# Optimization experiments

Measured on AMD Instinct MI355X. Metric: run time of the kernel, lower is better.

## Reference

```python
import jax, jax.numpy as jnp
from jax import lax
import numpy as np

E = 3            # num_experts
HEAD_CONV = 128  # head_conv
N_HEADS = 3      # hm, wh, reg
HEAD_CH = 2      # channels per head
BN_EPS = 1e-5


def _conv(x, w, stride, pad, groups=1):
    return lax.conv_general_dilated(
        x, w, (stride, stride), [(pad, pad), (pad, pad)],
        feature_group_count=groups,
        dimension_numbers=('NCHW', 'OIHW', 'NCHW'))


def _maxpool3s2p1(x):
    return lax.reduce_window(
        x, -jnp.inf, lax.max, (1, 1, 3, 3), (1, 1, 2, 2),
        ((0, 0), (0, 0), (1, 1), (1, 1)))


def setup_inputs() -> dict:
    key = jax.random.key(0)
    ks = jax.random.split(key, 8)
    B, C, T, H, W = 16, 3, 5, 384, 384
    s = 0.05
    inp = {
        'x': jax.random.normal(ks[0], (B, C, T, H, W), jnp.float32),
        # gating network params
        'g_conv_w': jax.random.normal(ks[1], (64, C * T, 7, 7), jnp.float32) * s,
        'g_bn_gamma': jnp.ones((64,), jnp.float32),
        'g_bn_beta': jnp.zeros((64,), jnp.float32),
        'g_bn_mean': jnp.zeros((64,), jnp.float32),
        'g_bn_var': jnp.ones((64,), jnp.float32),
        'g_fc_w': jax.random.normal(ks[2], (E, 64), jnp.float32) * s,
        'g_fc_b': jnp.zeros((E,), jnp.float32),
        # frozen expert params (stacked over expert dim E)
        'e_conv1_w': jax.random.normal(ks[3], (E, 64, C * T, 7, 7), jnp.float32) * s,
        'e_conv1_b': jnp.zeros((E, 64), jnp.float32),
        'e_head_w1': jax.random.normal(ks[4], (E, N_HEADS * HEAD_CONV, 64, 3, 3), jnp.float32) * s,
        'e_head_b1': jnp.zeros((E, N_HEADS * HEAD_CONV), jnp.float32),
        'e_head_w2': jax.random.normal(ks[5], (E, N_HEADS * HEAD_CH, HEAD_CONV, 1, 1), jnp.float32) * s,
        'e_head_b2': jnp.zeros((E, N_HEADS * HEAD_CH), jnp.float32),
    }
    return inp


def reference(x, g_conv_w, g_bn_gamma, g_bn_beta, g_bn_mean, g_bn_var,
              g_fc_w, g_fc_b, e_conv1_w, e_conv1_b,
              e_head_w1, e_head_b1, e_head_w2, e_head_b2):
    b, c, t, h, w = x.shape
    xr = x.reshape(b, c * t, h, w)

    # ---- ConvGatingNetwork ----
    f = _conv(xr, g_conv_w, 2, 3)                                  # [B,64,H/2,W/2]
    inv = g_bn_gamma / jnp.sqrt(g_bn_var + BN_EPS)
    f = f * inv[None, :, None, None] + (g_bn_beta - g_bn_mean * inv)[None, :, None, None]
    f = jax.nn.relu(f)
    f = _maxpool3s2p1(f)                                           # [B,64,H/4,W/4]
    feat = f.mean(axis=(2, 3))                                     # [B,64]
    logits = feat @ g_fc_w.T + g_fc_b                              # [B,E]
    idx = jnp.argmax(logits, axis=1)                               # top-1
    onehot = jax.nn.one_hot(idx, E, dtype=logits.dtype)            # [B,E]
    density = onehot.mean(axis=0)
    density_proxy = jax.nn.softmax(logits, axis=1).mean(axis=0)
    aux_loss = (density * density_proxy).sum() * E

    # ---- Experts (frozen DSFNet stand-in), computed densely then gathered ----
    def expert(cw, cb, hw1, hb1, hw2, hb2):
        y = jax.nn.relu(_conv(xr, cw, 4, 3) + cb[None, :, None, None])       # [B,64,H/4,W/4]
        y = jax.nn.relu(_conv(y, hw1, 1, 1) + hb1[None, :, None, None])      # [B,384,h,w]
        y = _conv(y, hw2, 1, 0, groups=N_HEADS) + hb2[None, :, None, None]   # [B,6,h,w]
        return y

    out_all = jax.vmap(expert)(e_conv1_w, e_conv1_b, e_head_w1, e_head_b1,
                               e_head_w2, e_head_b2)               # [E,B,6,h,w]
    out_all = lax.stop_gradient(out_all)  # experts frozen + torch.no_grad
    out = jnp.einsum('be,ebchw->bchw', onehot, out_all)            # per-sample top-1 gather
    return out, 0.01 * aux_loss
```

## Files before the change

kernel.cpp:

```cpp
#include <hip/hip_runtime.h>
#include <math.h>

#define BB 16
#define CIN 15
#define HW 384
#define XPL 147456
#define NX 35389440
#define PH 96
#define GW 192
#define YP 98
#define Y1IPL (98*98*64)
#define OUT_ELEMS (BB*6*PH*PH)

#define OFF_WG   0
#define OFF_WE1  122880
#define OFF_WH   491520
#define OFF_GSH  1818624
#define OFF_FEAT 1818880
#define OFF_IDX  1822976
#define OFF_CBUF 2097152

typedef __attribute__((ext_vector_type(8))) short short8;
typedef __attribute__((ext_vector_type(4))) float floatx4;
typedef __attribute__((ext_vector_type(4))) unsigned int uintx4;
typedef __attribute__((ext_vector_type(2))) unsigned int uintx2;

__device__ __forceinline__ unsigned bf16rne(float f) {
  unsigned u = __float_as_uint(f);
  unsigned r = ((u >> 16) & 1u) + 0x7FFFu;
  return (u + r) >> 16;
}
__device__ __forceinline__ float bf2f(unsigned short s) {
  return __uint_as_float(((unsigned)s) << 16);
}

__global__ __launch_bounds__(256) void k_prep(
    const float* __restrict__ g_conv_w, const float* __restrict__ e_conv1_w,
    const float* __restrict__ e_head_w1,
    const float* __restrict__ gamma, const float* __restrict__ var,
    const float* __restrict__ beta,  const float* __restrict__ mean,
    unsigned char* __restrict__ wsb)
{
  int i = blockIdx.x * 256 + threadIdx.x;
  unsigned short* Wg  = (unsigned short*)(wsb + OFF_WG);
  unsigned short* We1 = (unsigned short*)(wsb + OFF_WE1);
  unsigned short* Wh  = (unsigned short*)(wsb + OFF_WH);
  float* gsh = (float*)(wsb + OFF_GSH);
  if (i < 61440) {
    int j = i & 7, lane = (i >> 3) & 63, mtc = i >> 9;
    int mt = mtc & 3, c = mtc >> 2, ic = c >> 1, h = c & 1;
    int oc = mt * 16 + (lane & 15), q = lane >> 4;
    int ky = 4 * h + q, kx = j;
    float v = 0.f;
    if (ky < 7 && kx < 7) v = g_conv_w[oc * 735 + ic * 49 + ky * 7 + kx];
    float inv = gamma[oc] * rsqrtf(var[oc] + 1e-5f);
    Wg[i] = (unsigned short)bf16rne(v * inv);
  } else if (i < 245760) {
    int r = i - 61440;
    int e = r / 61440, r2 = r % 61440;
    int j = r2 & 7, lane = (r2 >> 3) & 63, mtc = r2 >> 9;
    int mt = mtc & 3, c = mtc >> 2, ic = c >> 1, h = c & 1;
    int oc = mt * 16 + (lane & 15), q = lane >> 4;
    int ky = 4 * h + q, kx = j;
    float v = 0.f;
    if (ky < 7 && kx < 7) v = e_conv1_w[(e * 64 + oc) * 735 + ic * 49 + ky * 7 + kx];
    We1[r] = (unsigned short)bf16rne(v);
  } else if (i < 909312) {
    int r = i - 245760;
    int e = r / 221184, r2 = r % 221184;
    int j = r2 & 7, lane = (r2 >> 3) & 63, mtc = r2 >> 9;
    int mt = mtc % 24, chunk = mtc / 24;
    int kk = chunk >> 1, ih = chunk & 1;
    int oc = mt * 16 + (lane & 15), q = lane >> 4;
    int ic = ih * 32 + q * 8 + j;
    Wh[r] = (unsigned short)bf16rne(e_head_w1[((e * 384 + oc) * 64 + ic) * 9 + kk]);
  } else if (i < 909376) {
    int oc = i - 909312;
    float inv = gamma[oc] * rsqrtf(var[oc] + 1e-5f);
    gsh[oc] = beta[oc] - mean[oc] * inv;
  }
}

__global__ __launch_bounds__(256) void k_gconv(
    const float* __restrict__ x, const unsigned short* __restrict__ Wg,
    const float* __restrict__ gsh, unsigned short* __restrict__ Cbuf)
{
  const int t = threadIdx.x, w = t >> 6, lane = t & 63, q = lane >> 4, ln = lane & 15;
  const int px0 = blockIdx.x * 16, py0 = blockIdx.y * 16, b = blockIdx.z;
  const int iy0 = 2 * py0 - 3, ix0 = 2 * px0 - 3;

  __shared__ unsigned tilU[11400];

  {
    const bool edge = (blockIdx.x == 0) | (blockIdx.x == 11) |
                      (blockIdx.y == 0) | (blockIdx.y == 11);
    const int xbase = b * CIN * XPL;
    if (!edge) {
      for (int it = 0; it < 5; ++it) {
        int i = it * 256 + t;
        if (i < 1140) {
          int half = i & 1, ri = i >> 1;
          int ic = ri / 38, row = ri - ic * 38;
          int iy = iy0 + row;
          int A = ix0 + 20 * half - 1;
          const float* src = x + xbase + ic * XPL + iy * HW + A;
          floatx4 F[6];
#pragma unroll
          for (int s = 0; s < 6; ++s) F[s] = *(const floatx4*)(src + 4 * s);
          float f[24];
#pragma unroll
          for (int s = 0; s < 6; ++s) {
            f[4*s] = F[s].x; f[4*s+1] = F[s].y; f[4*s+2] = F[s].z; f[4*s+3] = F[s].w;
          }
          unsigned* dst = tilU + ic * 760 + row * 20 + 10 * half;
#pragma unroll
          for (int jj = 0; jj < 5; ++jj) {
            uintx2 pr;
            pr.x = bf16rne(f[1 + 4*jj]) | (bf16rne(f[2 + 4*jj]) << 16);
            pr.y = bf16rne(f[3 + 4*jj]) | (bf16rne(f[4 + 4*jj]) << 16);
            *(uintx2*)(dst + 2 * jj) = pr;
          }
        }
      }
    } else {
      for (int it = 0; it < 5; ++it) {
        int i = it * 256 + t;
        if (i < 1140) {
          int half = i & 1, ri = i >> 1;
          int ic = ri / 38, row = ri - ic * 38;
          int iy = iy0 + row;
          unsigned rowm = (iy >= 0 && iy < HW) ? 0xFFFFFFFFu : 0u;
          int A = ix0 + 20 * half - 1;
          int a = xbase + ic * XPL + iy * HW + A;
          floatx4 F[6];
#pragma unroll
          for (int s = 0; s < 6; ++s) {
            int as = a + 4 * s;
            as = max(as, 0); as = min(as, NX - 4);
            F[s] = *(const floatx4*)(x + as);
          }
          float f[24];
#pragma unroll
          for (int s = 0; s < 6; ++s) {
            f[4*s] = F[s].x; f[4*s+1] = F[s].y; f[4*s+2] = F[s].z; f[4*s+3] = F[s].w;
          }
          unsigned* dst = tilU + ic * 760 + row * 20 + 10 * half;
#pragma unroll
          for (int jj = 0; jj < 5; ++jj) {
            uintx2 pr;
#pragma unroll
            for (int k = 0; k < 2; ++k) {
              int j = 2 * jj + k;
              int c = A + 1 + 2 * j;
              unsigned m = rowm;
              m &= ((c >= 0) && (c < HW)) ? 0xFFFFFFFFu : 0xFFFF0000u;
              m &= ((c + 1 >= 0) && (c + 1 < HW)) ? 0xFFFFFFFFu : 0x0000FFFFu;
              unsigned d = (bf16rne(f[1 + 2*j]) | (bf16rne(f[2 + 2*j]) << 16)) & m;
              if (k == 0) pr.x = d; else pr.y = d;
            }
            *(uintx2*)(dst + 2 * jj) = pr;
          }
        }
      }
    }
  }
  __syncthreads();

  floatx4 acc[4][4];
#pragma unroll
  for (int mt = 0; mt < 4; ++mt)
#pragma unroll
    for (int nt = 0; nt < 4; ++nt) acc[mt][nt] = 0.f;

#pragma unroll 3
  for (int ic = 0; ic < CIN; ++ic) {
#pragma unroll
    for (int h = 0; h < 2; ++h) {
      short8 af[4];
#pragma unroll
      for (int mt = 0; mt < 4; ++mt)
        af[mt] = *(const short8*)(Wg + (((ic * 2 + h) * 4 + mt) << 9) + lane * 8);
      short8 bf[4];
#pragma unroll
      for (int nt = 0; nt < 4; ++nt) {
        int row = 2 * (w * 4 + nt) + 4 * h + q;
        int bd = ic * 760 + row * 20 + ln;
        union { unsigned u[4]; short8 s; } cv;
        cv.u[0] = tilU[bd]; cv.u[1] = tilU[bd + 1];
        cv.u[2] = tilU[bd + 2]; cv.u[3] = tilU[bd + 3];
        bf[nt] = cv.s;
      }
#pragma unroll
      for (int mt = 0; mt < 4; ++mt)
#pragma unroll
        for (int nt = 0; nt < 4; ++nt)
          acc[mt][nt] = __builtin_amdgcn_mfma_f32_16x16x32_bf16(af[mt], bf[nt], acc[mt][nt], 0, 0, 0);
    }
  }

#pragma unroll
  for (int nt = 0; nt < 4; ++nt) {
    int py = py0 + w * 4 + nt, px = px0 + ln;
    size_t rowo = (((size_t)b * GW + py) * GW + px) * 64;
#pragma unroll
    for (int mt = 0; mt < 4; ++mt) {
      int ocb = mt * 16 + q * 4;
      float v0 = fmaxf(acc[mt][nt][0] + gsh[ocb + 0], 0.f);
      float v1 = fmaxf(acc[mt][nt][1] + gsh[ocb + 1], 0.f);
      float v2 = fmaxf(acc[mt][nt][2] + gsh[ocb + 2], 0.f);
      float v3 = fmaxf(acc[mt][nt][3] + gsh[ocb + 3], 0.f);
      uintx2 pr;
      pr.x = (bf16rne(v1) << 16) | bf16rne(v0);
      pr.y = (bf16rne(v3) << 16) | bf16rne(v2);
      *(uintx2*)(Cbuf + rowo + ocb) = pr;
    }
  }
}

__global__ __launch_bounds__(256) void k_pool(const unsigned short* __restrict__ Cb,
                                              float* __restrict__ feat)
{
  const int py = blockIdx.x, b = blockIdx.y;
  const int t = threadIdx.x, oc = t & 63, strip = t >> 6;
  const unsigned short* base = Cb + (size_t)b * GW * GW * 64 + oc;
  float sum = 0.f;
  for (int px = strip * 24; px < strip * 24 + 24; ++px) {
    float m = 0.f;
#pragma unroll
    for (int dy = 0; dy < 3; ++dy) {
      int row = 2 * py - 1 + dy;
      if (row < 0 || row >= GW) continue;
#pragma unroll
      for (int dx = 0; dx < 3; ++dx) {
        int col = 2 * px - 1 + dx;
        if (col < 0 || col >= GW) continue;
        m = fmaxf(m, bf2f(base[((size_t)row * GW + col) * 64]));
      }
    }
    sum += m;
  }
  __shared__ float red[4][64];
  red[strip][oc] = sum;
  __syncthreads();
  if (t < 64) {
    float s = red[0][oc] + red[1][oc] + red[2][oc] + red[3][oc];
    atomicAdd(&feat[b * 64 + oc], s);
  }
}

__global__ __launch_bounds__(64) void k_gate_fc(
    const float* __restrict__ feat, const float* __restrict__ fcw,
    const float* __restrict__ fcb, int* __restrict__ idxb,
    float* __restrict__ out_aux)
{
  __shared__ float sm[16][3];
  __shared__ int sidx[16];
  int t = threadIdx.x;
  if (t < 16) {
    float l[3];
#pragma unroll
    for (int e = 0; e < 3; ++e) {
      float s = fcb[e];
      for (int c = 0; c < 64; ++c)
        s = fmaf(feat[t * 64 + c] * (1.f / 9216.f), fcw[e * 64 + c], s);
      l[e] = s;
    }
    int best = 0; float bv = l[0];
    if (l[1] > bv) { bv = l[1]; best = 1; }
    if (l[2] > bv) { bv = l[2]; best = 2; }
    sidx[t] = best; idxb[t] = best;
    float mx = fmaxf(l[0], fmaxf(l[1], l[2]));
    float e0 = expf(l[0] - mx), e1 = expf(l[1] - mx), e2 = expf(l[2] - mx);
    float d = e0 + e1 + e2;
    sm[t][0] = e0 / d; sm[t][1] = e1 / d; sm[t][2] = e2 / d;
  }
  __syncthreads();
  if (t == 0) {
    float aux = 0.f;
    for (int e = 0; e < 3; ++e) {
      float cnt = 0.f, pr = 0.f;
      for (int b = 0; b < 16; ++b) { cnt += (sidx[b] == e) ? 1.f : 0.f; pr += sm[b][e]; }
      aux += (cnt / 16.f) * (pr / 16.f);
    }
    *out_aux = 0.01f * aux * 3.f;
  }
}

__global__ __launch_bounds__(256) void k_econv(
    const float* __restrict__ x, const unsigned short* __restrict__ We1,
    const float* __restrict__ biasp, const int* __restrict__ idxb,
    unsigned short* __restrict__ Y1)
{
  const int t = threadIdx.x, w = t >> 6, lane = t & 63, q = lane >> 4, ln = lane & 15;
  const int b = blockIdx.z;
  const int e = idxb[b];
  const unsigned short* W = We1 + e * 61440;
  const float* bs = biasp + e * 64;
  const int px0 = blockIdx.x * 16, py0 = blockIdx.y * 16;
  const int px = px0 + ln;

  const int c0 = 4 * px - 3;
  const int acol = c0 - 1;
  unsigned pm[4];
#pragma unroll
  for (int j = 0; j < 4; ++j) {
    int t0 = 2 * j, t1 = 2 * j + 1;
    unsigned m0 = (c0 + t0 >= 0 && c0 + t0 < HW) ? 0x0000FFFFu : 0u;
    unsigned m1 = (c0 + t1 >= 0 && c0 + t1 < HW) ? 0xFFFF0000u : 0u;
    pm[j] = m0 | m1;
  }

  int syq[4];
#pragma unroll
  for (int nt = 0; nt < 4; ++nt) syq[nt] = 4 * (py0 + w * 4 + nt) + q - 3;
  const int xbase = b * CIN * XPL;

  floatx4 acc[4][4];
#pragma unroll
  for (int mt = 0; mt < 4; ++mt)
#pragma unroll
    for (int nt = 0; nt < 4; ++nt) acc[mt][nt] = 0.f;

#pragma unroll 3
  for (int ic = 0; ic < CIN; ++ic) {
    const int icb = xbase + ic * XPL;
#pragma unroll
    for (int h = 0; h < 2; ++h) {
      short8 af[4];
#pragma unroll
      for (int mt = 0; mt < 4; ++mt)
        af[mt] = *(const short8*)(W + (((ic * 2 + h) * 4 + mt) << 9) + lane * 8);
      short8 bf[4];
#pragma unroll
      for (int nt = 0; nt < 4; ++nt) {
        int iy = syq[nt] + 4 * h;
        bool rv = (iy >= 0) && (iy < HW) && ((4 * h + q) < 7);
        int a0 = icb + iy * HW + acol;
        a0 = max(a0, 0); a0 = min(a0, NX - 12);
        const float* fp = x + a0;
        floatx4 fA = *(const floatx4*)(fp);
        floatx4 fB = *(const floatx4*)(fp + 4);
        floatx4 fC = *(const floatx4*)(fp + 8);
        float g[8];
        g[0] = fA.y; g[1] = fA.z; g[2] = fA.w; g[3] = fB.x;
        g[4] = fB.y; g[5] = fB.z; g[6] = fB.w; g[7] = fC.x;
        union { unsigned u[4]; short8 s; } cv;
#pragma unroll
        for (int j = 0; j < 4; ++j) {
          unsigned p = __builtin_amdgcn_perm(__float_as_uint(g[2 * j + 1]),
                                             __float_as_uint(g[2 * j]), 0x07060302u);
          p &= pm[j];
          cv.u[j] = rv ? p : 0u;
        }
        bf[nt] = cv.s;
      }
#pragma unroll
      for (int mt = 0; mt < 4; ++mt)
#pragma unroll
        for (int nt = 0; nt < 4; ++nt)
          acc[mt][nt] = __builtin_amdgcn_mfma_f32_16x16x32_bf16(af[mt], bf[nt], acc[mt][nt], 0, 0, 0);
    }
  }

#pragma unroll
  for (int nt = 0; nt < 4; ++nt) {
    int py = py0 + w * 4 + nt;
    size_t rowo = (((size_t)b * YP + py + 1) * YP + px + 1) * 64;
#pragma unroll
    for (int mt = 0; mt < 4; ++mt) {
      int ocb = mt * 16 + q * 4;
      float v0 = fmaxf(acc[mt][nt][0] + bs[ocb + 0], 0.f);
      float v1 = fmaxf(acc[mt][nt][1] + bs[ocb + 1], 0.f);
      float v2 = fmaxf(acc[mt][nt][2] + bs[ocb + 2], 0.f);
      float v3 = fmaxf(acc[mt][nt][3] + bs[ocb + 3], 0.f);
      uintx2 pr;
      pr.x = (bf16rne(v1) << 16) | bf16rne(v0);
      pr.y = (bf16rne(v3) << 16) | bf16rne(v2);
      *(uintx2*)(Y1 + rowo + ocb) = pr;
    }
  }
}

__global__ __launch_bounds__(256) void k_headm(
    const unsigned short* __restrict__ Y1, const unsigned short* __restrict__ Whp,
    const float* __restrict__ b1, const float* __restrict__ w2,
    const float* __restrict__ b2, const int* __restrict__ idxb,
    float* __restrict__ out)
{
  const int t = threadIdx.x, w = t >> 6, lane = t & 63, q = lane >> 4, ln = lane & 15;
  const int b = blockIdx.z, px0 = blockIdx.x * 16, py0 = blockIdx.y * 6;
  const int e = idxb[b];
  const unsigned short* W = Whp + e * 221184;

  __shared__ unsigned short patch[8 * 18 * 72];
  __shared__ float sred[6][4][16][6];

  {
    uintx4 vv[5];
#pragma unroll
    for (int r = 0; r < 5; ++r) {
      int i = r * 256 + t;
      if (i < 1152) {
        int row = i / 144, rem = i % 144, col = rem >> 3, s = rem & 7;
        vv[r] = *(const uintx4*)(Y1 + (((size_t)b * YP + py0 + row) * YP + (px0 + col)) * 64 + s * 8);
      }
    }
#pragma unroll
    for (int r = 0; r < 5; ++r) {
      int i = r * 256 + t;
      if (i < 1152) {
        int row = i / 144, rem = i % 144, col = rem >> 3, s = rem & 7;
        *(uintx4*)(patch + (row * 18 + col) * 72 + s * 8) = vv[r];
      }
    }
  }
  __syncthreads();

  floatx4 acc[6][6];
#pragma unroll
  for (int mt = 0; mt < 6; ++mt)
#pragma unroll
    for (int nt = 0; nt < 6; ++nt) acc[mt][nt] = 0.f;

#pragma unroll
  for (int kk = 0; kk < 9; ++kk) {
    const int ky = kk / 3, kx = kk % 3;
#pragma unroll
    for (int ih = 0; ih < 2; ++ih) {
      short8 bf[6];
#pragma unroll
      for (int nt = 0; nt < 6; ++nt) {
        int off = ((nt + ky) * 18 + (ln + kx)) * 72 + ih * 32 + q * 8;
        bf[nt] = *(const short8*)(patch + off);
      }
      const int cbase = ((kk * 2 + ih) * 24 + w * 6) << 9;
#pragma unroll
      for (int mt = 0; mt < 6; ++mt) {
        short8 af = *(const short8*)(W + cbase + (mt << 9) + lane * 8);
#pragma unroll
        for (int nt = 0; nt < 6; ++nt)
          acc[mt][nt] = __builtin_amdgcn_mfma_f32_16x16x32_bf16(af, bf[nt], acc[mt][nt], 0, 0, 0);
      }
    }
  }

#pragma unroll
  for (int nt = 0; nt < 6; ++nt) {
    float part[6] = {0.f, 0.f, 0.f, 0.f, 0.f, 0.f};
#pragma unroll
    for (int mt = 0; mt < 6; ++mt) {
      int ocb = w * 96 + mt * 16 + q * 4;
#pragma unroll
      for (int r = 0; r < 4; ++r) {
        int oc = ocb + r;
        float y = fmaxf(acc[mt][nt][r] + b1[e * 384 + oc], 0.f);
        int g = oc >> 7, kb = oc & 127;
        part[2 * g]     += y * w2[(e * 6 + 2 * g) * 128 + kb];
        part[2 * g + 1] += y * w2[(e * 6 + 2 * g + 1) * 128 + kb];
      }
    }
#pragma unroll
    for (int c = 0; c < 6; ++c) {
      part[c] += __shfl_down(part[c], 32);
      part[c] += __shfl_down(part[c], 16);
    }
    if (q == 0) {
#pragma unroll
      for (int c = 0; c < 6; ++c) sred[nt][w][ln][c] = part[c];
    }
  }
  __syncthreads();
  for (int i = t; i < 576; i += 256) {
    int pix = i / 6, c = i % 6;
    int nt = pix >> 4, pl = pix & 15;
    float s = sred[nt][0][pl][c] + sred[nt][1][pl][c] + sred[nt][2][pl][c] +
              sred[nt][3][pl][c] + b2[e * 6 + c];
    out[(((size_t)(b * 6 + c)) * PH + (py0 + nt)) * PH + (px0 + pl)] = s;
  }
}

extern "C" void kernel_launch(void* const* d_in, const int* in_sizes, int n_in,
                              void* d_out, int out_size, void* d_ws, size_t ws_size,
                              hipStream_t stream)
{
  const float* x         = (const float*)d_in[0];
  const float* g_fc_w    = (const float*)d_in[6];
  const float* g_fc_b    = (const float*)d_in[7];
  const float* e_conv1_b = (const float*)d_in[9];
  const float* e_head_b1 = (const float*)d_in[11];
  const float* e_head_w2 = (const float*)d_in[12];
  const float* e_head_b2 = (const float*)d_in[13];

  unsigned char* wsb = (unsigned char*)d_ws;
  unsigned short* Wg  = (unsigned short*)(wsb + OFF_WG);
  unsigned short* We1 = (unsigned short*)(wsb + OFF_WE1);
  unsigned short* Wh  = (unsigned short*)(wsb + OFF_WH);
  float* gsh  = (float*)(wsb + OFF_GSH);
  float* feat = (float*)(wsb + OFF_FEAT);
  int*   idxb = (int*)(wsb + OFF_IDX);
  unsigned short* Cbuf = (unsigned short*)(wsb + OFF_CBUF);
  unsigned short* Y1   = (unsigned short*)(wsb + OFF_CBUF);

  float* out = (float*)d_out;
  float* out_aux = out + OUT_ELEMS;

  hipMemsetAsync(feat, 0, 16 * 64 * sizeof(float), stream);
  hipLaunchKernelGGL(k_prep, dim3(3553), dim3(256), 0, stream,
                     (const float*)d_in[1], (const float*)d_in[8], (const float*)d_in[10],
                     (const float*)d_in[2], (const float*)d_in[5],
                     (const float*)d_in[3], (const float*)d_in[4], wsb);

  hipLaunchKernelGGL(k_gconv, dim3(12, 12, 16), dim3(256), 0, stream,
                     x, Wg, gsh, Cbuf);
  hipLaunchKernelGGL(k_pool, dim3(96, 16), dim3(256), 0, stream, Cbuf, feat);
  hipLaunchKernelGGL(k_gate_fc, dim3(1), dim3(64), 0, stream,
                     feat, g_fc_w, g_fc_b, idxb, out_aux);

  hipMemsetAsync(Y1, 0, (size_t)BB * Y1IPL * 2, stream);
  hipLaunchKernelGGL(k_econv, dim3(6, 6, 16), dim3(256), 0, stream,
                     x, We1, e_conv1_b, idxb, Y1);

  hipLaunchKernelGGL(k_headm, dim3(6, 16, 16), dim3(256), 0, stream,
                     Y1, Wh, e_head_b1, e_head_w2, e_head_b2, idxb, out);
}
```

Before: 663.4 us.

## Double-buffer head-conv weights into LDS via async global_load_lds in k_headm

The 3x3 head-conv kernel now stages its per-chunk weight fragments into a double-buffered LDS region using async global-to-LDS loads. Previously each wave read its A fragments straight from global memory. Each of the 18 K-chunks is split into two half-stages, and the next half is prefetched while MFMAs run on the current one. The LDS buffer is unioned with the reduction scratch. This replaces per-wave global weight loads, which were duplicated across waves and blocks, with shared LDS reads. The cost is 36 extra barriers with vmcnt waits per block, and more LDS that may reduce occupancy.

```diff
diff --git a/kernel.cpp b/kernel.cpp
--- a/kernel.cpp
+++ b/kernel.cpp
@@ -32,6 +32,13 @@
 }
 __device__ __forceinline__ float bf2f(unsigned short s) {
   return __uint_as_float(((unsigned)s) << 16);
+}
+
+__device__ __forceinline__ void gload_lds16(const unsigned short* g, unsigned short* l) {
+  __builtin_amdgcn_global_load_lds(
+      (const __attribute__((address_space(1))) unsigned int*)(const void*)g,
+      (__attribute__((address_space(3))) unsigned int*)(void*)l,
+      16, 0, 0);
 }
 
 __global__ __launch_bounds__(256) void k_prep(
@@ -393,7 +400,29 @@
   const unsigned short* W = Whp + e * 221184;
 
   __shared__ unsigned short patch[8 * 18 * 72];
-  __shared__ float sred[6][4][16][6];
+  __shared__ union SU {
+    unsigned short Wbuf[2 * 12 * 512];
+    float sred[6][4][16][6];
+  } su;
+
+  int soff[3], doff[3];
+#pragma unroll
+  for (int r = 0; r < 3; ++r) {
+    int g = r * 4 + w, wp = g / 3, mtp = g - wp * 3;
+    soff[r] = ((wp * 6 + mtp) << 9) + (lane << 3);
+    doff[r] = (g << 9) + (lane << 3);
+  }
+
+  auto stage = [&](int pn) {
+    int cs = pn >> 1, hs = pn & 1;
+    const unsigned short* srcb = W + ((cs * 24 + hs * 3) << 9);
+    unsigned short* dstb = su.Wbuf + hs * 6144;
+#pragma unroll
+    for (int r = 0; r < 3; ++r)
+      gload_lds16(srcb + soff[r], dstb + doff[r]);
+  };
+
+  stage(0);
 
   {
     uintx4 vv[5];
@@ -414,7 +443,8 @@
       }
     }
   }
-  __syncthreads();
+  asm volatile("s_waitcnt vmcnt(0) lgkmcnt(0)" ::: "memory");
+  __builtin_amdgcn_s_barrier();
 
   floatx4 acc[6][6];
 #pragma unroll
@@ -422,26 +452,43 @@
 #pragma unroll
     for (int nt = 0; nt < 6; ++nt) acc[mt][nt] = 0.f;
 
-#pragma unroll
-  for (int kk = 0; kk < 9; ++kk) {
-    const int ky = kk / 3, kx = kk % 3;
-#pragma unroll
-    for (int ih = 0; ih < 2; ++ih) {
-      short8 bf[6];
-#pragma unroll
-      for (int nt = 0; nt < 6; ++nt) {
-        int off = ((nt + ky) * 18 + (ln + kx)) * 72 + ih * 32 + q * 8;
-        bf[nt] = *(const short8*)(patch + off);
-      }
-      const int cbase = ((kk * 2 + ih) * 24 + w * 6) << 9;
-#pragma unroll
-      for (int mt = 0; mt < 6; ++mt) {
-        short8 af = *(const short8*)(W + cbase + (mt << 9) + lane * 8);
+  for (int chunk = 0; chunk < 18; ++chunk) {
+    const int kk = chunk >> 1, ih = chunk & 1;
+    const int ky = kk / 3, kx = kk - ky * 3;
+    short8 bfv[6];
+    stage(2 * chunk + 1);
+#pragma unroll
+    for (int nt = 0; nt < 6; ++nt) {
+      int off = ((nt + ky) * 18 + (ln + kx)) * 72 + ih * 32 + q * 8;
+      bfv[nt] = *(const short8*)(patch + off);
+    }
+    {
+      short8 afv[3];
+#pragma unroll
+      for (int m = 0; m < 3; ++m)
+        afv[m] = *(const short8*)(su.Wbuf + ((w * 3 + m) << 9) + (lane << 3));
+#pragma unroll
+      for (int m = 0; m < 3; ++m)
 #pragma unroll
         for (int nt = 0; nt < 6; ++nt)
-          acc[mt][nt] = __builtin_amdgcn_mfma_f32_16x16x32_bf16(af, bf[nt], acc[mt][nt], 0, 0, 0);
-      }
-    }
+          acc[m][nt] = __builtin_amdgcn_mfma_f32_16x16x32_bf16(afv[m], bfv[nt], acc[m][nt], 0, 0, 0);
+    }
+    asm volatile("s_waitcnt vmcnt(0)" ::: "memory");
+    __builtin_amdgcn_s_barrier();
+    if (chunk < 17) stage(2 * chunk + 2);
+    {
+      short8 afv[3];
+#pragma unroll
+      for (int m = 0; m < 3; ++m)
+        afv[m] = *(const short8*)(su.Wbuf + 6144 + ((w * 3 + m) << 9) + (lane << 3));
+#pragma unroll
+      for (int m = 0; m < 3; ++m)
+#pragma unroll
+        for (int nt = 0; nt < 6; ++nt)
+          acc[m + 3][nt] = __builtin_amdgcn_mfma_f32_16x16x32_bf16(afv[m], bfv[nt], acc[m + 3][nt], 0, 0, 0);
+    }
+    asm volatile("s_waitcnt vmcnt(0)" ::: "memory");
+    __builtin_amdgcn_s_barrier();
   }
 
 #pragma unroll
@@ -466,15 +513,15 @@
     }
     if (q == 0) {
 #pragma unroll
-      for (int c = 0; c < 6; ++c) sred[nt][w][ln][c] = part[c];
+      for (int c = 0; c < 6; ++c) su.sred[nt][w][ln][c] = part[c];
     }
   }
   __syncthreads();
   for (int i = t; i < 576; i += 256) {
     int pix = i / 6, c = i % 6;
     int nt = pix >> 4, pl = pix & 15;
-    float s = sred[nt][0][pl][c] + sred[nt][1][pl][c] + sred[nt][2][pl][c] +
-              sred[nt][3][pl][c] + b2[e * 6 + c];
+    float s = su.sred[nt][0][pl][c] + su.sred[nt][1][pl][c] + su.sred[nt][2][pl][c] +
+              su.sred[nt][3][pl][c] + b2[e * 6 + c];
     out[(((size_t)(b * 6 + c)) * PH + (py0 + nt)) * PH + (px0 + pl)] = s;
   }
 }
```

New measurement: 704.6 us. +6.2%, slower.
